# Kernel tuning notes

Measured on AMD Instinct MI355X. Metric: run time of the kernel, lower is better.

Reference implementation:

```python
import jax, jax.numpy as jnp
import numpy as np
import math

DIMS = 2560
N_HEADS = 32
ROT_DIM = 32  # partial rotary (Phi-2)
BASE = 10000.0
B, L = 1, 2048


def apply_rope(x, rot_dim=ROT_DIM, base=BASE, offset=0):
    # x: [B, H, L, hd]; rotate first rot_dim features, pass rest through
    Lx = x.shape[2]
    D = rot_dim // 2
    pos = jnp.arange(offset, offset + Lx, dtype=jnp.float32)              # [L]
    freq = jnp.exp(-jnp.arange(D, dtype=jnp.float32) * (math.log(base) / D))  # [D]
    theta = pos[:, None] * freq[None, :]                                   # [L, D]
    cos, sin = jnp.cos(theta), jnp.sin(theta)
    x1 = x[..., :D]
    x2 = x[..., D:rot_dim]
    rx1 = x1 * cos - x2 * sin
    rx2 = x1 * sin + x2 * cos
    return jnp.concatenate([rx1, rx2, x[..., rot_dim:]], axis=-1)


def setup_inputs() -> dict:
    key = jax.random.key(0)
    k1, k2, k3, k4, k5 = jax.random.split(key, 5)
    x = jax.random.normal(k1, (B, L, DIMS), dtype=jnp.float32)
    Wqkv_w = jax.random.normal(k2, (3 * DIMS, DIMS), dtype=jnp.float32) * 0.02
    Wqkv_b = jax.random.normal(k3, (3 * DIMS,), dtype=jnp.float32) * 0.02
    out_w = jax.random.normal(k4, (DIMS, DIMS), dtype=jnp.float32) * 0.02
    out_b = jax.random.normal(k5, (DIMS,), dtype=jnp.float32) * 0.02
    # additive causal mask, broadcast over batch/heads
    mask = jnp.triu(jnp.full((L, L), -1e9, dtype=jnp.float32), k=1)[None, None]
    return {"x": x, "Wqkv_w": Wqkv_w, "Wqkv_b": Wqkv_b,
            "out_w": out_w, "out_b": out_b, "mask": mask}


def reference(x, Wqkv_w, Wqkv_b, out_w, out_b, mask):
    Bx, Lx, _ = x.shape
    hd = DIMS // N_HEADS  # 80
    qkv = x @ Wqkv_w.T + Wqkv_b                          # [B, L, 3*dims]
    q, k, v = jnp.split(qkv, 3, axis=-1)
    def to_heads(t):
        return t.reshape(Bx, Lx, N_HEADS, hd).transpose(0, 2, 1, 3)  # [B,H,L,hd]
    q, k, v = to_heads(q), to_heads(k), to_heads(v)
    q = apply_rope(q)
    k = apply_rope(k)
    scale = 1.0 / math.sqrt(hd)
    scores = scale * jnp.einsum('bhqd,bhkd->bhqk', q, k) + mask  # [B,H,L,L]
    probs = jax.nn.softmax(scores, axis=-1)
    out = jnp.einsum('bhqk,bhkd->bhqd', probs, v)
    out = out.transpose(0, 2, 1, 3).reshape(Bx, Lx, DIMS)
    return out @ out_w.T + out_b
```

## Files before the change

### kernel.cpp

```cpp
#include <hip/hip_runtime.h>
#include <cstdint>
#include <cmath>

typedef __attribute__((ext_vector_type(4))) float f32x4;
typedef __attribute__((ext_vector_type(8))) short s16x8;

#define LOG2E 1.4426950408889634f

__device__ __forceinline__ unsigned short f2bf(float f) {
    unsigned int u = __float_as_uint(f);
    u += 0x7FFFu + ((u >> 16) & 1u);
    return (unsigned short)(u >> 16);
}
__device__ __forceinline__ float bf2f(unsigned short s) {
    return __uint_as_float(((unsigned int)s) << 16);
}

__device__ __forceinline__ void async_copy16(const void* g, void* l) {
    __builtin_amdgcn_global_load_lds(
        (const __attribute__((address_space(1))) unsigned int*)(uintptr_t)g,
        (__attribute__((address_space(3))) unsigned int*)(uintptr_t)l,
        16, 0, 0);
}

__global__ __launch_bounds__(256) void cast_bf16_kernel(const float* __restrict__ in,
                                                        unsigned short* __restrict__ out,
                                                        int n4) {
    int i = blockIdx.x * 256 + threadIdx.x;
    if (i < n4) {
        float4 v = ((const float4*)in)[i];
        ushort4 o;
        o.x = f2bf(v.x); o.y = f2bf(v.y); o.z = f2bf(v.z); o.w = f2bf(v.w);
        ((ushort4*)out)[i] = o;
    }
}

template <bool BF16_OUT>
__global__ __launch_bounds__(256) void gemm_bt(const unsigned short* __restrict__ A,
                                               const unsigned short* __restrict__ B,
                                               const float* __restrict__ bias,
                                               void* __restrict__ Cout,
                                               int M, int N, int K) {
    __shared__ unsigned short As[128 * 64];
    __shared__ unsigned short Bs[128 * 64];
    const int tid  = threadIdx.x;
    const int lane = tid & 63;
    const int wv   = tid >> 6;
    const int m0 = blockIdx.y * 128;
    const int n0 = blockIdx.x * 128;
    const int w_row = (wv >> 1) * 64;
    const int w_col = (wv & 1) * 64;
    const int fr = lane & 15;
    const int fg = lane >> 4;
    const int srow = lane >> 3;
    const int scol = ((lane & 7) ^ srow) * 8;
    const int rofs0 = ((fg ^ (fr & 7))) * 8;
    const int rofs1 = rofs0 ^ 32;

    f32x4 acc[4][4];
    const f32x4 zf = {0.f, 0.f, 0.f, 0.f};
    for (int r = 0; r < 4; ++r)
        for (int c = 0; c < 4; ++c) acc[r][c] = zf;

    const unsigned short* gA = A + (size_t)(m0 + wv * 32 + srow) * K + scol;
    const unsigned short* gB = B + (size_t)(n0 + wv * 32 + srow) * K + scol;
    const int ldsbase = (wv * 32 + srow) * 64;

    for (int k0 = 0; k0 < K; k0 += 64) {
        for (int i = 0; i < 4; ++i)
            async_copy16(gA + (size_t)i * 8 * K + k0, &As[(wv * 32 + i * 8) * 64]);
        for (int i = 0; i < 4; ++i)
            async_copy16(gB + (size_t)i * 8 * K + k0, &Bs[(wv * 32 + i * 8) * 64]);
        __syncthreads();
        {
            s16x8 af[4], bf[4];
            for (int r = 0; r < 4; ++r)
                af[r] = *(const s16x8*)&As[(w_row + r * 16 + fr) * 64 + rofs0];
            for (int c = 0; c < 4; ++c)
                bf[c] = *(const s16x8*)&Bs[(w_col + c * 16 + fr) * 64 + rofs0];
            for (int r = 0; r < 4; ++r)
                for (int c = 0; c < 4; ++c)
                    acc[r][c] = __builtin_amdgcn_mfma_f32_16x16x32_bf16(af[r], bf[c], acc[r][c], 0, 0, 0);
        }
        {
            s16x8 af[4], bf[4];
            for (int r = 0; r < 4; ++r)
                af[r] = *(const s16x8*)&As[(w_row + r * 16 + fr) * 64 + rofs1];
            for (int c = 0; c < 4; ++c)
                bf[c] = *(const s16x8*)&Bs[(w_col + c * 16 + fr) * 64 + rofs1];
            for (int r = 0; r < 4; ++r)
                for (int c = 0; c < 4; ++c)
                    acc[r][c] = __builtin_amdgcn_mfma_f32_16x16x32_bf16(af[r], bf[c], acc[r][c], 0, 0, 0);
        }
        __syncthreads();
    }

    const int rb = (lane >> 4) * 4;
    for (int c = 0; c < 4; ++c) {
        int col = n0 + w_col + c * 16 + fr;
        float bv = bias[col];
        for (int r = 0; r < 4; ++r) {
            int row = m0 + w_row + r * 16 + rb;
            for (int q = 0; q < 4; ++q) {
                float v = acc[r][c][q] + bv;
                if constexpr (BF16_OUT)
                    ((unsigned short*)Cout)[(size_t)(row + q) * N + col] = f2bf(v);
                else
                    ((float*)Cout)[(size_t)(row + q) * N + col] = v;
            }
        }
    }
}

__global__ __launch_bounds__(256) void rope_q_kernel(unsigned short* __restrict__ qkv) {
    int g = blockIdx.x * 256 + threadIdx.x;
    int c = g & 1;
    int h = (g >> 1) & 31;
    int p = g >> 6;
    size_t base = (size_t)p * 7680 + h * 80 + c * 8;
    s16x8 x1v = *(const s16x8*)(qkv + base);
    s16x8 x2v = *(const s16x8*)(qkv + base + 16);
    s16x8 o1, o2;
    for (int j = 0; j < 8; ++j) {
        int dp = c * 8 + j;
        float freq = expf(-(float)dp * 0.57564627324851142f);
        float sn, cs;
        sincosf((float)p * freq, &sn, &cs);
        float x1 = bf2f((unsigned short)x1v[j]);
        float x2 = bf2f((unsigned short)x2v[j]);
        o1[j] = (short)f2bf(x1 * cs - x2 * sn);
        o2[j] = (short)f2bf(x1 * sn + x2 * cs);
    }
    *(s16x8*)(qkv + base)      = o1;
    *(s16x8*)(qkv + base + 16) = o2;
}

__global__ __launch_bounds__(256) void rope_pack_k_kernel(const unsigned short* __restrict__ qkv,
                                                          unsigned short* __restrict__ Kp) {
    int g = blockIdx.x * 256 + threadIdx.x;
    int c   = g % 12;
    int h   = (g / 12) & 31;
    int pos = g / 384;
    int d0 = c * 8;
    const unsigned short* kb = qkv + (size_t)pos * 7680 + 2560 + h * 80;
    s16x8 v = {0, 0, 0, 0, 0, 0, 0, 0};
    if (c >= 4) {
        if (d0 < 80) v = *(const s16x8*)(kb + d0);
    } else if (c < 2) {
        s16x8 x1v = *(const s16x8*)(kb + d0);
        s16x8 x2v = *(const s16x8*)(kb + d0 + 16);
        for (int j = 0; j < 8; ++j) {
            int dp = d0 + j;
            float freq = expf(-(float)dp * 0.57564627324851142f);
            float sn, cs;
            sincosf((float)pos * freq, &sn, &cs);
            v[j] = (short)f2bf(bf2f((unsigned short)x1v[j]) * cs -
                               bf2f((unsigned short)x2v[j]) * sn);
        }
    } else {
        s16x8 x1v = *(const s16x8*)(kb + d0 - 16);
        s16x8 x2v = *(const s16x8*)(kb + d0);
        for (int j = 0; j < 8; ++j) {
            int dp = d0 - 16 + j;
            float freq = expf(-(float)dp * 0.57564627324851142f);
            float sn, cs;
            sincosf((float)pos * freq, &sn, &cs);
            v[j] = (short)f2bf(bf2f((unsigned short)x1v[j]) * sn +
                               bf2f((unsigned short)x2v[j]) * cs);
        }
    }
    *(s16x8*)(Kp + ((size_t)h * 2048 + pos) * 96 + d0) = v;
}

__global__ __launch_bounds__(256) void pack_v_kernel(const unsigned short* __restrict__ qkv,
                                                     unsigned short* __restrict__ Vp) {
    int h  = blockIdx.x & 31;
    int g64 = blockIdx.x >> 5;
    int k0 = g64 * 64;
    int tid = threadIdx.x;
    for (int ci = tid; ci < 320; ci += 256) {
        int d   = ci % 80;
        int kbl = ci / 80;
        unsigned short tmp[16];
        for (int j = 0; j < 16; ++j)
            tmp[j] = qkv[(size_t)(k0 + kbl * 16 + j) * 7680 + 5120 + h * 80 + d];
        unsigned short* dst = Vp + ((size_t)h * 128 + g64 * 4 + kbl) * 1280 + d * 16;
        *(s16x8*)dst       = *(const s16x8*)&tmp[0];
        *(s16x8*)(dst + 8) = *(const s16x8*)&tmp[8];
    }
}

__global__ __launch_bounds__(256) void flash3_kernel(const unsigned short* __restrict__ qkv,
                                                     const unsigned short* __restrict__ Kp,
                                                     const unsigned short* __restrict__ Vp,
                                                     unsigned short* __restrict__ attn) {
    __shared__ unsigned short Pt[4][640];
    __shared__ float parts[2][16][84];
    __shared__ float parts_l[2][16];
    const int tid  = threadIdx.x;
    const int lane = tid & 63;
    const int wv   = tid >> 6;
    const int h = blockIdx.x & 31;
    const int p = blockIdx.x >> 5;
    const int s    = (wv < 2) ? p : (127 - p);
    const int j    = wv & 1;
    const int slot = wv >> 1;
    const int fr = lane & 15;
    const int fg = lane >> 4;
    const float k1 = 0.11180339887498949f * LOG2E;
    const int sm16 = s * 16;

    const int n    = s + 1;
    const int half = (n + 1) >> 1;
    const int kstart = (j ? half : 0) * 16;
    const int kend   = (j ? n : half) * 16;

    s16x8 qf[3];
    {
        const unsigned short* qb = qkv + (size_t)(sm16 + fr) * 7680 + h * 80;
        const s16x8 zs = {0, 0, 0, 0, 0, 0, 0, 0};
        for (int sd = 0; sd < 3; ++sd) {
            int d = 32 * sd + fg * 8;
            qf[sd] = (d < 80) ? *(const s16x8*)(qb + d) : zs;
        }
    }

    f32x4 O[5];
    const f32x4 zf = {0.f, 0.f, 0.f, 0.f};
    for (int t = 0; t < 5; ++t) O[t] = zf;
    float rs[4] = {0.f, 0.f, 0.f, 0.f};

    const unsigned short* kptr = Kp + (size_t)h * 2048 * 96 + (size_t)(kstart + fr) * 96 + fg * 8;
    const unsigned short* vptr = Vp + (size_t)h * 128 * 1280 + (size_t)(kstart >> 4) * 1280
                                 + (fg >> 1) * 1280 + fr * 16 + (fg & 1) * 8;
    unsigned short* Pw = &Pt[wv][0];

    for (int k0 = kstart; k0 < kend; k0 += 32) {
        s16x8 kb[2][3];
        for (int g = 0; g < 2; ++g)
            for (int sd = 0; sd < 3; ++sd)
                kb[g][sd] = *(const s16x8*)(kptr + g * 1536 + sd * 32);
        s16x8 vb[5];
        for (int t = 0; t < 5; ++t)
            vb[t] = *(const s16x8*)(vptr + t * 256);

        f32x4 sa[2] = {zf, zf};
        for (int g = 0; g < 2; ++g)
            for (int sd = 0; sd < 3; ++sd)
                sa[g] = __builtin_amdgcn_mfma_f32_16x16x32_bf16(qf[sd], kb[g][sd], sa[g], 0, 0, 0);

        if (k0 + 32 > sm16 || k0 + 32 > kend) {
            for (int g = 0; g < 2; ++g)
                for (int r = 0; r < 4; ++r) {
                    int key  = k0 + g * 16 + fr;
                    int qrow = sm16 + fg * 4 + r;
                    if (key > qrow || key >= kend) sa[g][r] = -1e30f;
                }
        }

        float pr[2][4];
        for (int g = 0; g < 2; ++g)
            for (int r = 0; r < 4; ++r)
                pr[g][r] = __builtin_amdgcn_exp2f(sa[g][r] * k1);
        for (int r = 0; r < 4; ++r) rs[r] += pr[0][r] + pr[1][r];
        for (int g = 0; g < 2; ++g)
            for (int r = 0; r < 4; ++r)
                Pw[(fg * 4 + r) * 40 + g * 16 + fr] =
                    (unsigned short)(__float_as_uint(pr[g][r]) >> 16);

        s16x8 pa = *(const s16x8*)(Pw + fr * 40 + fg * 8);
        for (int t = 0; t < 5; ++t)
            O[t] = __builtin_amdgcn_mfma_f32_16x16x32_bf16(pa, vb[t], O[t], 0, 0, 0);

        kptr += 3072;
        vptr += 2560;
    }

    for (int r = 0; r < 4; ++r) {
        float v = rs[r];
        v += __shfl_xor(v, 1);
        v += __shfl_xor(v, 2);
        v += __shfl_xor(v, 4);
        v += __shfl_xor(v, 8);
        rs[r] = v;
    }

    if (j) {
        for (int t = 0; t < 5; ++t)
            for (int r = 0; r < 4; ++r)
                parts[slot][fg * 4 + r][t * 16 + fr] = O[t][r];
        if (fr == 0)
            for (int r = 0; r < 4; ++r) parts_l[slot][fg * 4 + r] = rs[r];
    }
    __syncthreads();
    if (!j) {
        for (int r = 0; r < 4; ++r) {
            float rl = 1.0f / (rs[r] + parts_l[slot][fg * 4 + r]);
            int row = sm16 + fg * 4 + r;
            for (int t = 0; t < 5; ++t) {
                float v = (O[t][r] + parts[slot][fg * 4 + r][t * 16 + fr]) * rl;
                attn[(size_t)row * 2560 + h * 80 + t * 16 + fr] = f2bf(v);
            }
        }
    }
}

extern "C" void kernel_launch(void* const* d_in, const int* in_sizes, int n_in,
                              void* d_out, int out_size, void* d_ws, size_t ws_size,
                              hipStream_t stream) {
    const float* x    = (const float*)d_in[0];
    const float* wqkv = (const float*)d_in[1];
    const float* bqkv = (const float*)d_in[2];
    const float* outw = (const float*)d_in[3];
    const float* outb = (const float*)d_in[4];

    unsigned short* xb    = (unsigned short*)d_ws;
    unsigned short* wqkvb = xb + (size_t)2048 * 2560;
    unsigned short* Kp    = wqkvb;
    unsigned short* Vp    = wqkvb + (size_t)32 * 2048 * 96;
    unsigned short* outwb = wqkvb + (size_t)7680 * 2560;
    unsigned short* qkvb  = outwb + (size_t)2560 * 2560;
    unsigned short* attnb = qkvb  + (size_t)2048 * 7680;
    float* out = (float*)d_out;

    cast_bf16_kernel<<<2048 * 2560 / 4 / 256, 256, 0, stream>>>(x, xb, 2048 * 2560 / 4);
    cast_bf16_kernel<<<7680 * 2560 / 4 / 256, 256, 0, stream>>>(wqkv, wqkvb, 7680 * 2560 / 4);
    cast_bf16_kernel<<<2560 * 2560 / 4 / 256, 256, 0, stream>>>(outw, outwb, 2560 * 2560 / 4);

    gemm_bt<true><<<dim3(7680 / 128, 2048 / 128), 256, 0, stream>>>(
        xb, wqkvb, bqkv, (void*)qkvb, 2048, 7680, 2560);

    rope_q_kernel<<<2048 * 64 / 256, 256, 0, stream>>>(qkvb);
    rope_pack_k_kernel<<<2048 * 384 / 256, 256, 0, stream>>>(qkvb, Kp);
    pack_v_kernel<<<32 * 32, 256, 0, stream>>>(qkvb, Vp);

    flash3_kernel<<<2048, 256, 0, stream>>>(qkvb, Kp, Vp, attnb);

    gemm_bt<false><<<dim3(2560 / 128, 2048 / 128), 256, 0, stream>>>(
        attnb, outwb, outb, (void*)out, 2048, 2560, 2560);
}
```

Before: 442.1 us.

## Replace QKV GEMM with 256x256 tiled, double-buffered, phase-interleaved MFMA kernel

Measured after the change: 416.5 us. 5.8% less time.

```diff
diff --git a/kernel.cpp b/kernel.cpp
--- a/kernel.cpp
+++ b/kernel.cpp
@@ -64,7 +64,6 @@
 
     const unsigned short* gA = A + (size_t)(m0 + wv * 32 + srow) * K + scol;
     const unsigned short* gB = B + (size_t)(n0 + wv * 32 + srow) * K + scol;
-    const int ldsbase = (wv * 32 + srow) * 64;
 
     for (int k0 = 0; k0 < K; k0 += 64) {
         for (int i = 0; i < 4; ++i)
@@ -107,6 +106,148 @@
                     ((unsigned short*)Cout)[(size_t)(row + q) * N + col] = f2bf(v);
                 else
                     ((float*)Cout)[(size_t)(row + q) * N + col] = v;
+            }
+        }
+    }
+}
+
+
+#define BAR()   __builtin_amdgcn_s_barrier()
+#define LGKM0() asm volatile("s_waitcnt lgkmcnt(0)" ::: "memory")
+#define VMW(N)  asm volatile("s_waitcnt vmcnt(" #N ")" ::: "memory")
+
+#define STAGE2(gXb, XsBuf, rb, kk) \
+    async_copy16(gXb + (size_t)(rb) * K + (kk), (void*)&XsBuf[(rb) * 64])
+
+#define ST_AS0(b, kk) { STAGE2(gAb, As[b], rbA_0, kk);      STAGE2(gAb, As[b], rbA_1, kk); }
+#define ST_AS1(b, kk) { STAGE2(gAb, As[b], rbA_0 + 64, kk); STAGE2(gAb, As[b], rbA_1 + 64, kk); }
+#define ST_BS0(b, kk) { STAGE2(gBb, Bs[b], rbB_0, kk);      STAGE2(gBb, Bs[b], rbB_1, kk); }
+#define ST_BS1(b, kk) { STAGE2(gBb, Bs[b], rbB_0 + 32, kk); STAGE2(gBb, Bs[b], rbB_1 + 32, kk); }
+
+#define READ_A(b, mh) \
+    _Pragma("unroll") \
+    for (int mm_ = 0; mm_ < 4; ++mm_) { \
+        const unsigned short* ap_ = &As[b][(wr * 128 + (mh) * 64 + mm_ * 16 + fr) * 64]; \
+        Ar[mm_][0] = *(const s16x8*)(ap_ + rofs0); \
+        Ar[mm_][1] = *(const s16x8*)(ap_ + rofs1); \
+    }
+
+#define READ_B(b, nh, Brg) \
+    _Pragma("unroll") \
+    for (int nn_ = 0; nn_ < 2; ++nn_) { \
+        const unsigned short* bp_ = &Bs[b][(wc * 64 + (nh) * 32 + nn_ * 16 + fr) * 64]; \
+        Brg[nn_][0] = *(const s16x8*)(bp_ + rofs0); \
+        Brg[nn_][1] = *(const s16x8*)(bp_ + rofs1); \
+    }
+
+#define MFMA_Q(mh, nh, Brg) \
+    _Pragma("unroll") \
+    for (int mm_ = 0; mm_ < 4; ++mm_) { \
+        _Pragma("unroll") \
+        for (int nn_ = 0; nn_ < 2; ++nn_) { \
+            acc[(mh) * 4 + mm_][(nh) * 2 + nn_] = __builtin_amdgcn_mfma_f32_16x16x32_bf16( \
+                Ar[mm_][0], Brg[nn_][0], acc[(mh) * 4 + mm_][(nh) * 2 + nn_], 0, 0, 0); \
+            acc[(mh) * 4 + mm_][(nh) * 2 + nn_] = __builtin_amdgcn_mfma_f32_16x16x32_bf16( \
+                Ar[mm_][1], Brg[nn_][1], acc[(mh) * 4 + mm_][(nh) * 2 + nn_], 0, 0, 0); \
+        } \
+    }
+
+#define GROUP(b, t) { \
+    int x1_ = (t) + 1; if (x1_ >= ktiles) x1_ -= ktiles; \
+    int x2_ = (t) + 2; if (x2_ >= ktiles) x2_ -= ktiles; \
+    const int kn1 = x1_ << 6; \
+    const int kn2 = x2_ << 6; \
+     \
+    READ_A(b, 0); \
+    READ_B(b, 0, Br0); \
+    ST_AS1((b) ^ 1, kn1); \
+    BAR(); LGKM0(); \
+    __builtin_amdgcn_s_setprio(1); MFMA_Q(0, 0, Br0); __builtin_amdgcn_s_setprio(0); \
+    BAR(); \
+     \
+    READ_B(b, 1, Br1); \
+    ST_AS0(b, kn2); \
+    BAR(); LGKM0(); \
+    __builtin_amdgcn_s_setprio(1); MFMA_Q(0, 1, Br1); __builtin_amdgcn_s_setprio(0); \
+    BAR(); \
+     \
+    READ_A(b, 1); \
+    ST_BS0(b, kn2); \
+    BAR(); LGKM0(); \
+    __builtin_amdgcn_s_setprio(1); MFMA_Q(1, 0, Br0); __builtin_amdgcn_s_setprio(0); \
+    BAR(); \
+     \
+    ST_BS1(b, kn2); \
+    BAR(); \
+    __builtin_amdgcn_s_setprio(1); MFMA_Q(1, 1, Br1); __builtin_amdgcn_s_setprio(0); \
+    VMW(6); \
+    BAR(); \
+}
+
+__global__ __launch_bounds__(512, 2) void gemm256_bt(const unsigned short* __restrict__ A,
+                                                     const unsigned short* __restrict__ B,
+                                                     const float* __restrict__ bias,
+                                                     unsigned short* __restrict__ C,
+                                                     int M, int N, int K) {
+    __shared__ unsigned short As[2][256 * 64];
+    __shared__ unsigned short Bs[2][256 * 64];
+    const int tid  = threadIdx.x;
+    const int lane = tid & 63;
+    const int wv   = tid >> 6;
+    const int wr   = wv >> 2;
+    const int wc   = wv & 3;
+    const int by = blockIdx.x & 7;
+    const int bx = blockIdx.x >> 3;
+    const int m0 = by * 256;
+    const int n0 = bx * 256;
+    const int fr = lane & 15;
+    const int fg = lane >> 4;
+    const int rofs0 = (fg ^ (fr & 7)) * 8;
+    const int rofs1 = rofs0 ^ 32;
+    const int rlane = lane >> 3;
+    const int swzc  = ((lane & 7) ^ (rlane & 7)) * 8;
+    const int idx0 = wv * 2, idx1 = wv * 2 + 1;
+    const int rbA_0 = idx0 * 8 + ((idx0 >= 8) ? 64 : 0);
+    const int rbA_1 = idx1 * 8 + ((idx1 >= 8) ? 64 : 0);
+    const int rbB_0 = (idx0 >> 2) * 64 + (idx0 & 3) * 8;
+    const int rbB_1 = (idx1 >> 2) * 64 + (idx1 & 3) * 8;
+    const int ktiles = K >> 6;
+
+    const unsigned short* gAb = A + (size_t)(m0 + rlane) * K + swzc;
+    const unsigned short* gBb = B + (size_t)(n0 + rlane) * K + swzc;
+
+    f32x4 acc[8][4];
+    const f32x4 zf = {0.f, 0.f, 0.f, 0.f};
+#pragma unroll
+    for (int i = 0; i < 8; ++i)
+#pragma unroll
+        for (int j = 0; j < 4; ++j) acc[i][j] = zf;
+
+    s16x8 Ar[4][2], Br0[2][2], Br1[2][2];
+
+    ST_AS0(0, 0); ST_AS1(0, 0); ST_BS0(0, 0); ST_BS1(0, 0);
+    ST_AS0(1, 64); ST_BS0(1, 64); ST_BS1(1, 64);
+    VMW(6);
+    BAR();
+
+    const int nit = ktiles >> 1;
+    for (int it = 0; it < nit; ++it) {
+        GROUP(0, it * 2);
+        GROUP(1, it * 2 + 1);
+    }
+
+    const int rb = (lane >> 4) * 4;
+#pragma unroll
+    for (int nn = 0; nn < 4; ++nn) {
+        int col = n0 + wc * 64 + nn * 16 + fr;
+        float bv = bias[col];
+#pragma unroll
+        for (int mm = 0; mm < 8; ++mm) {
+            int row = m0 + wr * 128 + mm * 16 + rb;
+#pragma unroll
+            for (int q = 0; q < 4; ++q) {
+                float v = acc[mm][nn][q] + bv;
+                C[(size_t)(row + q) * N + col] = f2bf(v);
             }
         }
     }
@@ -327,8 +468,7 @@
     cast_bf16_kernel<<<7680 * 2560 / 4 / 256, 256, 0, stream>>>(wqkv, wqkvb, 7680 * 2560 / 4);
     cast_bf16_kernel<<<2560 * 2560 / 4 / 256, 256, 0, stream>>>(outw, outwb, 2560 * 2560 / 4);
 
-    gemm_bt<true><<<dim3(7680 / 128, 2048 / 128), 256, 0, stream>>>(
-        xb, wqkvb, bqkv, (void*)qkvb, 2048, 7680, 2560);
+    gemm256_bt<<<240, 512, 0, stream>>>(xb, wqkvb, bqkv, qkvb, 2048, 7680, 2560);
 
     rope_q_kernel<<<2048 * 64 / 256, 256, 0, stream>>>(qkvb);
     rope_pack_k_kernel<<<2048 * 384 / 256, 256, 0, stream>>>(qkvb, Kp);
```
